# Performance work log

Hardware: AMD Instinct MI355X
Metric: run time of the kernel (lower is better)

The kernel has to match this reference:

```python
import jax, jax.numpy as jnp
import numpy as np

BN_EPS = 1e-5

def setup_inputs() -> dict:
    key = jax.random.key(0)
    ks = jax.random.split(key, 6)
    B, C, H, W, K = 16, 512, 64, 64, 32
    return {
        "x": jax.random.normal(ks[0], (B, C, H, W), dtype=jnp.float32),
        "conv_w": jax.random.normal(ks[1], (C, C), dtype=jnp.float32) * (1.0 / np.sqrt(C)),
        "conv_b": jax.random.normal(ks[2], (C,), dtype=jnp.float32) * 0.01,
        "codewords": jax.random.normal(ks[3], (K, C), dtype=jnp.float32) * (1.0 / np.sqrt(C)),
        "scale": jax.random.uniform(ks[4], (K,), dtype=jnp.float32, minval=-1.0, maxval=0.0),
        "bn_gamma": jnp.ones((K,), jnp.float32),
        "bn_beta": jnp.zeros((K,), jnp.float32),
        "bn_mean": jnp.zeros((K,), jnp.float32),
        "bn_var": jnp.ones((K,), jnp.float32),
        "fc_w": jax.random.normal(ks[5], (C, C), dtype=jnp.float32) * (1.0 / np.sqrt(C)),
        "fc_b": jnp.zeros((C,), jnp.float32),
    }

def reference(x, conv_w, conv_b, codewords, scale, bn_gamma, bn_beta, bn_mean, bn_var, fc_w, fc_b):
    B, C, H, W = x.shape
    N = H * W
    # 1x1 conv projection: (B,C,H,W) x (O,C) -> (B,O,H,W)
    proj = jnp.einsum('bchw,oc->bohw', x, conv_w) + conv_b[None, :, None, None]
    z = proj.reshape(B, C, N).transpose(0, 2, 1)  # (B, N, C)
    # scaled L2 distances without materializing (B,N,K,C):
    # ||z - cw||^2 = ||z||^2 - 2 z.cw + ||cw||^2
    z_sq = jnp.sum(z * z, axis=-1)                     # (B, N)
    cw_sq = jnp.sum(codewords * codewords, axis=-1)    # (K,)
    cross = jnp.einsum('bnc,kc->bnk', z, codewords)    # (B, N, K)
    dist = scale[None, None, :] * (z_sq[:, :, None] - 2.0 * cross + cw_sq[None, None, :])
    assign = jax.nn.softmax(dist, axis=2)              # (B, N, K)
    # aggregate: sum_n a[b,n,k] * (z[b,n,c] - cw[k,c])
    enc = jnp.einsum('bnk,bnc->bkc', assign, z) - jnp.sum(assign, axis=1)[:, :, None] * codewords[None]  # (B, K, C)
    # BatchNorm1d(num_codes) in eval mode normalizes the K (feature) axis, then ReLU
    inv_std = jax.lax.rsqrt(bn_var + BN_EPS)
    enc_bn = (enc - bn_mean[None, :, None]) * (inv_std * bn_gamma)[None, :, None] + bn_beta[None, :, None]
    encoding_feat = jnp.mean(jax.nn.relu(enc_bn), axis=1)  # (B, C)
    # sigmoid channel gate + residual fuse
    gamma = jax.nn.sigmoid(encoding_feat @ fc_w.T + fc_b)  # (B, C)
    y = gamma[:, :, None, None]
    output = jax.nn.relu(x + x * y)
    return (encoding_feat, output)
```

## Files before the change

kernel.cpp:

```cpp
#include <hip/hip_runtime.h>
#include <hip/hip_bf16.h>
#include <stdint.h>

#define DEV static __device__ __forceinline__

typedef __attribute__((ext_vector_type(8))) short bf16x8;
typedef __attribute__((ext_vector_type(4))) float f32x4;

DEV void async_ld16(const void* g, void* l) {
  __builtin_amdgcn_global_load_lds(
      (const __attribute__((address_space(1))) void*)g,
      (__attribute__((address_space(3))) void*)l, 16, 0, 0);
}

DEV unsigned short f2bf(float f) {
  union { __hip_bfloat16 h; unsigned short u; } c;
  c.h = __float2bfloat16(f);
  return c.u;
}

#define Bb 16
#define Cc 512
#define Nn 4096
#define Kk 32
#define NSPLIT 32

__global__ void k_castw(const float* __restrict__ a, __hip_bfloat16* __restrict__ o) {
  int i = blockIdx.x * 256 + threadIdx.x;
  o[i] = __float2bfloat16(a[i]);
}

__global__ void k_cw(const float* __restrict__ cw, __hip_bfloat16* __restrict__ cwb,
                     float* __restrict__ cwsq) {
  int k = blockIdx.x, lane = threadIdx.x;
  float s = 0.f;
#pragma unroll
  for (int j = 0; j < 8; ++j) {
    float v = cw[k * Cc + lane * 8 + j];
    cwb[k * Cc + lane * 8 + j] = __float2bfloat16(v);
    s += v * v;
  }
  for (int off = 32; off; off >>= 1) s += __shfl_down(s, off);
  if (lane == 0) cwsq[k] = s;
}

__global__ __launch_bounds__(256) void k_gemm_z(const float* __restrict__ X,
                                                const __hip_bfloat16* __restrict__ Bw,
                                                const float* __restrict__ bias,
                                                __hip_bfloat16* __restrict__ Z) {
  constexpr int LDA = 36;
  constexpr int AE = 128 * LDA;
  constexpr int BE = 128 * 32;
  __shared__ __align__(16) unsigned short As[2 * AE];
  __shared__ __align__(16) __hip_bfloat16 Bs[2 * BE];
  const int b = blockIdx.y;
  const int n0 = (blockIdx.x & 31) * 128;
  const int c0 = (blockIdx.x >> 5) * 128;
  const int tid = threadIdx.x;
  const int lane = tid & 63, wid = tid >> 6;
  const int wr = (wid >> 1) * 64, wc = (wid & 1) * 64;
  const int cg = tid >> 5;
  const int ng = tid & 31;
  const float* Xb = X + (size_t)b * Cc * Nn + n0 + ng * 4;
  const __hip_bfloat16* Bbp = Bw + (size_t)c0 * Cc;
  f32x4 acc[4][4] = {};
  float4 av[4];
#pragma unroll
  for (int i = 0; i < 4; ++i)
    av[i] = *(const float4*)&Xb[(size_t)(cg * 4 + i) * Nn];
#pragma unroll
  for (int j = 0; j < 2; ++j) {
    int li = tid + j * 256;
    int row = li >> 2;
    int kc = ((li & 3) ^ ((li >> 3) & 3)) * 8;
    async_ld16(Bbp + (size_t)row * Cc + kc, (char*)Bs + li * 16);
  }
  int cur = 0;
  for (int kt = 0; kt < 16; ++kt) {
    unsigned short* Aw = As + cur * AE;
    int slot = cg ^ (ng & 7);
#pragma unroll
    for (int j = 0; j < 4; ++j) {
      int n = ng * 4 + j;
      ushort4 w;
      w.x = f2bf(av[0][j]);
      w.y = f2bf(av[1][j]);
      w.z = f2bf(av[2][j]);
      w.w = f2bf(av[3][j]);
      *(ushort4*)&Aw[n * LDA + slot * 4] = w;
    }
    __syncthreads();
    if (kt < 15) {
      char* Bwr = (char*)(Bs + (cur ^ 1) * BE);
#pragma unroll
      for (int j = 0; j < 2; ++j) {
        int li = tid + j * 256;
        int row = li >> 2;
        int kc = ((li & 3) ^ ((li >> 3) & 3)) * 8;
        async_ld16(Bbp + (size_t)row * Cc + (kt + 1) * 32 + kc, Bwr + li * 16);
      }
#pragma unroll
      for (int i = 0; i < 4; ++i)
        av[i] = *(const float4*)&Xb[(size_t)((kt + 1) * 32 + cg * 4 + i) * Nn];
    }
    const unsigned short* Ar = As + cur * AE;
    const __hip_bfloat16* Br = Bs + cur * BE;
    bf16x8 af[4], bfv[4];
#pragma unroll
    for (int m = 0; m < 4; ++m) {
      int row = wr + m * 16 + (lane & 15);
      int h = (row >> 2) & 7;
      int g = lane >> 4;
      int s0 = (2 * g) ^ h, s1 = (2 * g + 1) ^ h;
      union { ushort4 u2[2]; bf16x8 v8; } t;
      t.u2[0] = *(const ushort4*)&Ar[row * LDA + s0 * 4];
      t.u2[1] = *(const ushort4*)&Ar[row * LDA + s1 * 4];
      af[m] = t.v8;
    }
#pragma unroll
    for (int nf = 0; nf < 4; ++nf) {
      int row = wc + nf * 16 + (lane & 15);
      int q = (lane >> 4) ^ ((row >> 1) & 3);
      bfv[nf] = *(const bf16x8*)&Br[row * 32 + q * 8];
    }
#pragma unroll
    for (int m = 0; m < 4; ++m)
#pragma unroll
      for (int nf = 0; nf < 4; ++nf)
        acc[m][nf] = __builtin_amdgcn_mfma_f32_16x16x32_bf16(af[m], bfv[nf], acc[m][nf], 0, 0, 0);
    cur ^= 1;
  }
  __hip_bfloat16* Zb = Z + ((size_t)b * Nn + n0) * Cc + c0;
#pragma unroll
  for (int nf = 0; nf < 4; ++nf) {
    int col = wc + nf * 16 + (lane & 15);
    float bv = bias[c0 + col];
#pragma unroll
    for (int m = 0; m < 4; ++m) {
#pragma unroll
      for (int r = 0; r < 4; ++r) {
        int row = wr + m * 16 + (lane >> 4) * 4 + r;
        Zb[(size_t)row * Cc + col] = __float2bfloat16(acc[m][nf][r] + bv);
      }
    }
  }
}

__global__ __launch_bounds__(256) void k_cross(const __hip_bfloat16* __restrict__ Z,
                                               const __hip_bfloat16* __restrict__ CW,
                                               const float* __restrict__ scale,
                                               const float* __restrict__ cwsq,
                                               float* __restrict__ assign,
                                               float* __restrict__ asum) {
  __shared__ __align__(16) __hip_bfloat16 As[128 * 32];
  __shared__ __align__(16) __hip_bfloat16 Bs[32 * 32];
  __shared__ float s_zsq[128];
  __shared__ float s_asum[Kk];
  int b = blockIdx.y;
  int n0 = blockIdx.x * 128;
  int tid = threadIdx.x, lane = tid & 63, wid = tid >> 6;
  if (tid < Kk) s_asum[tid] = 0.f;
  const __hip_bfloat16* Ab = Z + ((size_t)b * Nn + n0) * Cc;
  f32x4 acc[2][2] = {};
  float sq = 0.f;
  for (int kt = 0; kt < 16; ++kt) {
    int k0 = kt * 32;
    __syncthreads();
#pragma unroll
    for (int j = 0; j < 2; ++j) {
      int li = tid + j * 256;
      int row = li >> 2;
      int kc = ((li & 3) ^ ((li >> 3) & 3)) * 8;
      async_ld16(Ab + (size_t)row * Cc + k0 + kc, (char*)As + li * 16);
    }
    if (tid < 128) {
      int row = tid >> 2;
      int kc = ((tid & 3) ^ ((tid >> 3) & 3)) * 8;
      async_ld16(CW + (size_t)row * Cc + k0 + kc, (char*)Bs + tid * 16);
    }
    __syncthreads();
    {
      int row = tid >> 1, h = tid & 1;
      int rsw = (row >> 1) & 3;
#pragma unroll
      for (int c8 = 0; c8 < 2; ++c8) {
        union { bf16x8 v; __hip_bfloat16 e[8]; } t;
        t.v = *(const bf16x8*)&As[row * 32 + (((2 * h + c8) ^ rsw) * 8)];
#pragma unroll
        for (int i = 0; i < 8; ++i) {
          float v = __bfloat162float(t.e[i]);
          sq += v * v;
        }
      }
    }
    bf16x8 af[2], bfv[2];
#pragma unroll
    for (int m = 0; m < 2; ++m) {
      int row = wid * 32 + m * 16 + (lane & 15);
      int q = (lane >> 4) ^ ((row >> 1) & 3);
      af[m] = *(const bf16x8*)&As[row * 32 + q * 8];
    }
#pragma unroll
    for (int nf = 0; nf < 2; ++nf) {
      int row = nf * 16 + (lane & 15);
      int q = (lane >> 4) ^ ((row >> 1) & 3);
      bfv[nf] = *(const bf16x8*)&Bs[row * 32 + q * 8];
    }
#pragma unroll
    for (int m = 0; m < 2; ++m)
#pragma unroll
      for (int nf = 0; nf < 2; ++nf)
        acc[m][nf] = __builtin_amdgcn_mfma_f32_16x16x32_bf16(af[m], bfv[nf], acc[m][nf], 0, 0, 0);
  }
  sq += __shfl_xor(sq, 1);
  if ((tid & 1) == 0) s_zsq[tid >> 1] = sq;
  __syncthreads();
  float sc[2], cq[2];
#pragma unroll
  for (int nf = 0; nf < 2; ++nf) {
    sc[nf] = scale[nf * 16 + (lane & 15)];
    cq[nf] = cwsq[nf * 16 + (lane & 15)];
  }
  float asump0 = 0.f, asump1 = 0.f;
#pragma unroll
  for (int m = 0; m < 2; ++m) {
#pragma unroll
    for (int r = 0; r < 4; ++r) {
      int row = wid * 32 + m * 16 + (lane >> 4) * 4 + r;
      float zq = s_zsq[row];
      float v0 = sc[0] * (zq - 2.f * acc[m][0][r] + cq[0]);
      float v1 = sc[1] * (zq - 2.f * acc[m][1][r] + cq[1]);
      float mx = fmaxf(v0, v1);
#pragma unroll
      for (int off = 1; off < 16; off <<= 1) mx = fmaxf(mx, __shfl_xor(mx, off));
      float e0 = __expf(v0 - mx), e1 = __expf(v1 - mx);
      float s = e0 + e1;
#pragma unroll
      for (int off = 1; off < 16; off <<= 1) s += __shfl_xor(s, off);
      float inv = 1.f / s;
      float a0 = e0 * inv, a1 = e1 * inv;
      acc[m][0][r] = a0;
      acc[m][1][r] = a1;
      asump0 += a0;
      asump1 += a1;
    }
  }
  asump0 += __shfl_xor(asump0, 16); asump0 += __shfl_xor(asump0, 32);
  asump1 += __shfl_xor(asump1, 16); asump1 += __shfl_xor(asump1, 32);
  if (lane < 16) {
    atomicAdd(&s_asum[lane], asump0);
    atomicAdd(&s_asum[16 + lane], asump1);
  }
  float* Cb = assign + ((size_t)b * Nn + n0) * Kk;
#pragma unroll
  for (int m = 0; m < 2; ++m)
#pragma unroll
    for (int nf = 0; nf < 2; ++nf) {
      int col = nf * 16 + (lane & 15);
#pragma unroll
      for (int r = 0; r < 4; ++r) {
        int row = wid * 32 + m * 16 + (lane >> 4) * 4 + r;
        Cb[(size_t)row * Kk + col] = acc[m][nf][r];
      }
    }
  __syncthreads();
  if (tid < Kk) atomicAdd(&asum[b * Kk + tid], s_asum[tid]);
}

__global__ __launch_bounds__(256) void k_enc_part(const float* __restrict__ assign,
                                                  const __hip_bfloat16* __restrict__ Z,
                                                  float* __restrict__ part) {
  __shared__ float sa[128][Kk];
  int b = blockIdx.z;
  int s = blockIdx.y;
  int c = blockIdx.x * 256 + threadIdx.x;
  int tid = threadIdx.x;
  int n0 = s * 128;
  const float* ap = assign + ((size_t)b * Nn + n0) * Kk;
  for (int i = tid; i < 128 * Kk; i += 256) sa[i >> 5][i & 31] = ap[i];
  __syncthreads();
  float acc[Kk];
#pragma unroll
  for (int k = 0; k < Kk; ++k) acc[k] = 0.f;
  const __hip_bfloat16* zp = Z + ((size_t)b * Nn + n0) * Cc + c;
  for (int n = 0; n < 128; ++n) {
    float zv = __bfloat162float(zp[(size_t)n * Cc]);
    const float4* sp = (const float4*)&sa[n][0];
#pragma unroll
    for (int q = 0; q < 8; ++q) {
      float4 a4 = sp[q];
      acc[4 * q + 0] = fmaf(a4.x, zv, acc[4 * q + 0]);
      acc[4 * q + 1] = fmaf(a4.y, zv, acc[4 * q + 1]);
      acc[4 * q + 2] = fmaf(a4.z, zv, acc[4 * q + 2]);
      acc[4 * q + 3] = fmaf(a4.w, zv, acc[4 * q + 3]);
    }
  }
  float* pp = part + (((size_t)s * Bb + b) * Kk) * Cc + c;
#pragma unroll
  for (int k = 0; k < Kk; ++k) pp[(size_t)k * Cc] = acc[k];
}

__global__ __launch_bounds__(256) void k_enc_bn(const float* __restrict__ part,
                                                const float* __restrict__ asum,
                                                const float* __restrict__ cw,
                                                const float* __restrict__ bn_g,
                                                const float* __restrict__ bn_b,
                                                const float* __restrict__ bn_m,
                                                const float* __restrict__ bn_v,
                                                float* __restrict__ ef) {
  int bk = blockIdx.x;
  int b = bk >> 5, k = bk & 31;
  int tid = threadIdx.x;
  float g = bn_g[k], bt = bn_b[k], mn = bn_m[k], iv = rsqrtf(bn_v[k] + 1e-5f);
  float as = asum[bk];
  for (int c = tid; c < Cc; c += 256) {
    float e = 0.f;
#pragma unroll
    for (int s = 0; s < NSPLIT; ++s)
      e += part[(((size_t)s * Bb + b) * Kk + k) * Cc + c];
    e -= as * cw[k * Cc + c];
    e = (e - mn) * (iv * g) + bt;
    e = fmaxf(e, 0.f);
    atomicAdd(&ef[b * Cc + c], e * (1.f / 32.f));
  }
}

__global__ void k_fc(const float* __restrict__ ef, const float* __restrict__ fcw,
                     const float* __restrict__ fcb, float* __restrict__ gamma) {
  int b = blockIdx.x;
  int o = blockIdx.y * 4 + (threadIdx.x >> 6);
  int lane = threadIdx.x & 63;
  const float* w = fcw + (size_t)o * Cc;
  const float* e = ef + b * Cc;
  float s = 0.f;
#pragma unroll
  for (int j = 0; j < 8; ++j) s += e[lane + j * 64] * w[lane + j * 64];
  for (int off = 32; off; off >>= 1) s += __shfl_down(s, off);
  if (lane == 0) gamma[b * Cc + o] = 1.f / (1.f + __expf(-(s + fcb[o])));
}

__global__ __launch_bounds__(256) void k_out(const float* __restrict__ x,
                                             const float* __restrict__ gamma,
                                             float* __restrict__ out) {
  int bc = blockIdx.x;
  float m = 1.f + gamma[bc];
  size_t base = (size_t)bc * (Nn / 4);
  const float4* xp = (const float4*)x + base;
  float4* op = (float4*)out + base;
#pragma unroll
  for (int j = 0; j < 4; ++j) {
    int i = j * 256 + threadIdx.x;
    float4 v = xp[i];
    float4 r;
    r.x = fmaxf(v.x * m, 0.f);
    r.y = fmaxf(v.y * m, 0.f);
    r.z = fmaxf(v.z * m, 0.f);
    r.w = fmaxf(v.w * m, 0.f);
    op[i] = r;
  }
}

extern "C" void kernel_launch(void* const* d_in, const int* in_sizes, int n_in,
                              void* d_out, int out_size, void* d_ws, size_t ws_size,
                              hipStream_t stream) {
  const float* x = (const float*)d_in[0];
  const float* conv_w = (const float*)d_in[1];
  const float* conv_b = (const float*)d_in[2];
  const float* codewords = (const float*)d_in[3];
  const float* scale = (const float*)d_in[4];
  const float* bn_gamma = (const float*)d_in[5];
  const float* bn_beta = (const float*)d_in[6];
  const float* bn_mean = (const float*)d_in[7];
  const float* bn_var = (const float*)d_in[8];
  const float* fc_w = (const float*)d_in[9];
  const float* fc_b = (const float*)d_in[10];

  float* ef_out = (float*)d_out;
  float* out = (float*)d_out + Bb * Cc;

  char* ws = (char*)d_ws;
  size_t off = 0;
  float* part = (float*)(ws + off);
  off += (size_t)NSPLIT * Bb * Kk * Cc * 4;
  __hip_bfloat16* z = (__hip_bfloat16*)(ws + off);
  off += (size_t)Bb * Nn * Cc * 2;
  float* assign = (float*)(ws + off);
  off += (size_t)Bb * Nn * Kk * 4;
  __hip_bfloat16* wbf = (__hip_bfloat16*)(ws + off);
  off += (size_t)Cc * Cc * 2;
  __hip_bfloat16* cwb = (__hip_bfloat16*)(ws + off);
  off += (size_t)Kk * Cc * 2;
  float* cwsq = (float*)(ws + off);
  off += 512;
  float* asum = (float*)(ws + off);
  off += (size_t)Bb * Kk * 4;
  float* gamma = (float*)(ws + off);
  off += (size_t)Bb * Cc * 4;
  (void)ws_size; (void)n_in; (void)in_sizes; (void)out_size;

  hipMemsetAsync(asum, 0, Bb * Kk * 4, stream);
  hipMemsetAsync(ef_out, 0, Bb * Cc * 4, stream);

  k_castw<<<dim3(Cc * Cc / 256), dim3(256), 0, stream>>>(conv_w, wbf);
  k_cw<<<dim3(Kk), dim3(64), 0, stream>>>(codewords, cwb, cwsq);
  k_gemm_z<<<dim3((Nn / 128) * 4, Bb), dim3(256), 0, stream>>>(x, wbf, conv_b, z);
  k_cross<<<dim3(Nn / 128, Bb), dim3(256), 0, stream>>>(z, cwb, scale, cwsq, assign, asum);
  k_enc_part<<<dim3(Cc / 256, NSPLIT, Bb), dim3(256), 0, stream>>>(assign, z, part);
  k_enc_bn<<<dim3(Bb * Kk), dim3(256), 0, stream>>>(part, asum, codewords, bn_gamma, bn_beta,
                                                    bn_mean, bn_var, ef_out);
  k_fc<<<dim3(Bb, Cc / 4), dim3(256), 0, stream>>>(ef_out, fc_w, fc_b, gamma);
  k_out<<<dim3(Bb * Cc), dim3(256), 0, stream>>>(x, gamma, out);
}
```

Before: 189.2 us.

## Double-buffer k_cross LDS tiles and halve encoder split count

In k_cross, the shared-memory tiles for Z and codewords are double-buffered, so the async load of the next K-slice is issued while the current slice is consumed, with one barrier per iteration instead of two. This aims to hide global-load latency behind the MFMA and sum-of-squares work. Separately, NSPLIT drops from 32 to 16 and k_enc_part handles 256 rows per block instead of 128. That halves the partial-sum buffer and reduction traffic but launches fewer blocks and uses more LDS per block.

```diff
diff --git a/kernel.cpp b/kernel.cpp
--- a/kernel.cpp
+++ b/kernel.cpp
@@ -23,7 +23,7 @@
 #define Cc 512
 #define Nn 4096
 #define Kk 32
-#define NSPLIT 32
+#define NSPLIT 16
 
 __global__ void k_castw(const float* __restrict__ a, __hip_bfloat16* __restrict__ o) {
   int i = blockIdx.x * 256 + threadIdx.x;
@@ -152,8 +152,10 @@
                                                const float* __restrict__ cwsq,
                                                float* __restrict__ assign,
                                                float* __restrict__ asum) {
-  __shared__ __align__(16) __hip_bfloat16 As[128 * 32];
-  __shared__ __align__(16) __hip_bfloat16 Bs[32 * 32];
+  constexpr int AE = 128 * 32;
+  constexpr int BE = 32 * 32;
+  __shared__ __align__(16) __hip_bfloat16 As[2 * AE];
+  __shared__ __align__(16) __hip_bfloat16 Bs[2 * BE];
   __shared__ float s_zsq[128];
   __shared__ float s_asum[Kk];
   int b = blockIdx.y;
@@ -163,29 +165,46 @@
   const __hip_bfloat16* Ab = Z + ((size_t)b * Nn + n0) * Cc;
   f32x4 acc[2][2] = {};
   float sq = 0.f;
+#pragma unroll
+  for (int j = 0; j < 2; ++j) {
+    int li = tid + j * 256;
+    int row = li >> 2;
+    int kc = ((li & 3) ^ ((li >> 3) & 3)) * 8;
+    async_ld16(Ab + (size_t)row * Cc + kc, (char*)As + li * 16);
+  }
+  if (tid < 128) {
+    int row = tid >> 2;
+    int kc = ((tid & 3) ^ ((tid >> 3) & 3)) * 8;
+    async_ld16(CW + (size_t)row * Cc + kc, (char*)Bs + tid * 16);
+  }
+  int cur = 0;
   for (int kt = 0; kt < 16; ++kt) {
-    int k0 = kt * 32;
     __syncthreads();
-#pragma unroll
-    for (int j = 0; j < 2; ++j) {
-      int li = tid + j * 256;
-      int row = li >> 2;
-      int kc = ((li & 3) ^ ((li >> 3) & 3)) * 8;
-      async_ld16(Ab + (size_t)row * Cc + k0 + kc, (char*)As + li * 16);
-    }
-    if (tid < 128) {
-      int row = tid >> 2;
-      int kc = ((tid & 3) ^ ((tid >> 3) & 3)) * 8;
-      async_ld16(CW + (size_t)row * Cc + k0 + kc, (char*)Bs + tid * 16);
-    }
-    __syncthreads();
+    if (kt < 15) {
+      int k0 = (kt + 1) * 32;
+      char* Awr = (char*)(As + (cur ^ 1) * AE);
+#pragma unroll
+      for (int j = 0; j < 2; ++j) {
+        int li = tid + j * 256;
+        int row = li >> 2;
+        int kc = ((li & 3) ^ ((li >> 3) & 3)) * 8;
+        async_ld16(Ab + (size_t)row * Cc + k0 + kc, Awr + li * 16);
+      }
+      if (tid < 128) {
+        int row = tid >> 2;
+        int kc = ((tid & 3) ^ ((tid >> 3) & 3)) * 8;
+        async_ld16(CW + (size_t)row * Cc + k0 + kc, (char*)(Bs + (cur ^ 1) * BE) + tid * 16);
+      }
+    }
+    const __hip_bfloat16* Ar = As + cur * AE;
+    const __hip_bfloat16* Br = Bs + cur * BE;
     {
       int row = tid >> 1, h = tid & 1;
       int rsw = (row >> 1) & 3;
 #pragma unroll
       for (int c8 = 0; c8 < 2; ++c8) {
         union { bf16x8 v; __hip_bfloat16 e[8]; } t;
-        t.v = *(const bf16x8*)&As[row * 32 + (((2 * h + c8) ^ rsw) * 8)];
+        t.v = *(const bf16x8*)&Ar[row * 32 + (((2 * h + c8) ^ rsw) * 8)];
 #pragma unroll
         for (int i = 0; i < 8; ++i) {
           float v = __bfloat162float(t.e[i]);
@@ -198,19 +217,20 @@
     for (int m = 0; m < 2; ++m) {
       int row = wid * 32 + m * 16 + (lane & 15);
       int q = (lane >> 4) ^ ((row >> 1) & 3);
-      af[m] = *(const bf16x8*)&As[row * 32 + q * 8];
+      af[m] = *(const bf16x8*)&Ar[row * 32 + q * 8];
     }
 #pragma unroll
     for (int nf = 0; nf < 2; ++nf) {
       int row = nf * 16 + (lane & 15);
       int q = (lane >> 4) ^ ((row >> 1) & 3);
-      bfv[nf] = *(const bf16x8*)&Bs[row * 32 + q * 8];
+      bfv[nf] = *(const bf16x8*)&Br[row * 32 + q * 8];
     }
 #pragma unroll
     for (int m = 0; m < 2; ++m)
 #pragma unroll
       for (int nf = 0; nf < 2; ++nf)
         acc[m][nf] = __builtin_amdgcn_mfma_f32_16x16x32_bf16(af[m], bfv[nf], acc[m][nf], 0, 0, 0);
+    cur ^= 1;
   }
   sq += __shfl_xor(sq, 1);
   if ((tid & 1) == 0) s_zsq[tid >> 1] = sq;
@@ -270,20 +290,20 @@
 __global__ __launch_bounds__(256) void k_enc_part(const float* __restrict__ assign,
                                                   const __hip_bfloat16* __restrict__ Z,
                                                   float* __restrict__ part) {
-  __shared__ float sa[128][Kk];
+  __shared__ float sa[256][Kk];
   int b = blockIdx.z;
   int s = blockIdx.y;
   int c = blockIdx.x * 256 + threadIdx.x;
   int tid = threadIdx.x;
-  int n0 = s * 128;
+  int n0 = s * 256;
   const float* ap = assign + ((size_t)b * Nn + n0) * Kk;
-  for (int i = tid; i < 128 * Kk; i += 256) sa[i >> 5][i & 31] = ap[i];
+  for (int i = tid; i < 256 * Kk; i += 256) sa[i >> 5][i & 31] = ap[i];
   __syncthreads();
   float acc[Kk];
 #pragma unroll
   for (int k = 0; k < Kk; ++k) acc[k] = 0.f;
   const __hip_bfloat16* zp = Z + ((size_t)b * Nn + n0) * Cc + c;
-  for (int n = 0; n < 128; ++n) {
+  for (int n = 0; n < 256; ++n) {
     float zv = __bfloat162float(zp[(size_t)n * Cc]);
     const float4* sp = (const float4*)&sa[n][0];
 #pragma unroll
```

Measured after the change: 203.0 us. 7.3% more time.
